# Optimization experiments

Measured on AMD Instinct MI355X. Metric: run time of the kernel, lower is better.

The kernel has to match this reference:

```python
import math
import jax, jax.numpy as jnp
import numpy as np

EMB = 1024
HEADS = 16
EXPAND = 2
HEAD_D = EMB // HEADS * EXPAND  # 128
N, S = 2, 2048


def setup_inputs() -> dict:
    key = jax.random.key(0)
    ks = jax.random.split(key, 10)
    lim = 1.0 / math.sqrt(EMB)  # nn.Linear default init range
    inp = {
        "query": jax.random.normal(ks[0], (N, S, EMB), dtype=jnp.float32),
        "key": jax.random.normal(ks[1], (N, S, EMB), dtype=jnp.float32),
        "value": jax.random.normal(ks[2], (N, S, EMB), dtype=jnp.float32),
        "mask": jax.random.randint(ks[3], (1, S, S), 0, 2, dtype=jnp.int32),
        "Wq": jax.random.uniform(ks[4], (EMB * EXPAND, EMB), jnp.float32, -lim, lim),
        "bq": jax.random.uniform(ks[5], (EMB * EXPAND,), jnp.float32, -lim, lim),
        "Wk": jax.random.uniform(ks[6], (EMB * EXPAND, EMB), jnp.float32, -lim, lim),
        "bk": jax.random.uniform(ks[7], (EMB * EXPAND,), jnp.float32, -lim, lim),
        "Wv": jax.random.uniform(ks[8], (EMB * EXPAND, EMB), jnp.float32, -lim, lim),
        "bv": jax.random.uniform(ks[9], (EMB * EXPAND,), jnp.float32, -lim, lim),
    }
    return inp


def _split_heads(x):
    # (N, S, H*D) -> (N, H, S, D)
    n, s, _ = x.shape
    return x.reshape(n, s, HEADS, HEAD_D).transpose(0, 2, 1, 3)


def reference(query, key, value, mask, Wq, bq, Wk, bk, Wv, bv):
    Q = _split_heads(jax.nn.relu(query @ Wq.T + bq))  # (N,H,S,D)
    K = _split_heads(jax.nn.relu(key @ Wk.T + bk))
    V = _split_heads(jax.nn.relu(value @ Wv.T + bv))
    scale = 1.0 / math.sqrt(HEAD_D)
    scores = jnp.einsum("nhqd,nhkd->nhqk", Q, K) * scale  # (N,H,S,S)
    scores = jnp.where(mask[None, :, :, :] == 0, jnp.float32(-1e7), scores)
    probs = jax.nn.softmax(scores, axis=-1)
    y = jnp.einsum("nhqk,nhkd->nhqd", probs, V)  # (N,H,S,D)
    return y.transpose(0, 2, 1, 3).reshape(query.shape[0], S, HEADS * HEAD_D)
```

## Files before the change

kernel.cpp:

```cpp
#include <hip/hip_runtime.h>

typedef __bf16 bf16;
typedef __bf16 bf16x8 __attribute__((ext_vector_type(8)));
typedef __bf16 bf16x4 __attribute__((ext_vector_type(4)));
typedef float f32x4 __attribute__((ext_vector_type(4)));

#define MFMA_BF16(A, B, C) __builtin_amdgcn_mfma_f32_16x16x32_bf16((A), (B), (C), 0, 0, 0)

#define EMB 1024
#define ODIM 2048
#define SEQ 2048
#define HEADS 16
#define HD 128

__device__ __forceinline__ void gload16(const bf16* g, const bf16* l) {
  __builtin_amdgcn_global_load_lds(
      (const __attribute__((address_space(1))) unsigned int*)(const void*)g,
      (__attribute__((address_space(3))) unsigned int*)(void*)l, 16, 0, 0);
}

__global__ __launch_bounds__(256) void cvt_bf16_k(const float* __restrict__ q,
                                                  const float* __restrict__ k,
                                                  const float* __restrict__ v,
                                                  const float* __restrict__ Wq,
                                                  const float* __restrict__ Wk,
                                                  const float* __restrict__ Wv,
                                                  bf16* __restrict__ Xall,
                                                  bf16* __restrict__ Wall) {
  const unsigned XV = 4096u * 1024u / 8u;
  const unsigned WV = 2048u * 1024u / 8u;
  unsigned id = blockIdx.x * 256 + threadIdx.x;
  const float* src;
  bf16* dst;
  size_t off;
  if (id < 3 * XV) {
    unsigned p = id / XV;
    off = (size_t)(id - p * XV) * 8;
    src = (p == 0) ? q : (p == 1 ? k : v);
    dst = Xall + (size_t)p * (4096u * 1024u);
  } else {
    unsigned id2 = id - 3 * XV;
    unsigned p = id2 / WV;
    off = (size_t)(id2 - p * WV) * 8;
    src = (p == 0) ? Wq : (p == 1 ? Wk : Wv);
    dst = Wall + (size_t)p * (2048u * 1024u);
  }
  float4 a = *(const float4*)(src + off);
  float4 b = *(const float4*)(src + off + 4);
  bf16x8 o;
  o[0] = (bf16)a.x; o[1] = (bf16)a.y; o[2] = (bf16)a.z; o[3] = (bf16)a.w;
  o[4] = (bf16)b.x; o[5] = (bf16)b.y; o[6] = (bf16)b.z; o[7] = (bf16)b.w;
  *(bf16x8*)(dst + off) = o;
}

__global__ __launch_bounds__(256) void build_maskbits_k(const int* __restrict__ mask,
                                                        unsigned long long* __restrict__ mb) {
  int w = blockIdx.x * 256 + threadIdx.x;
  int q = w >> 5, c = w & 31;
  const int4* m4 = reinterpret_cast<const int4*>(mask + (size_t)q * SEQ + c * 64);
  unsigned long long bits = 0ull;
#pragma unroll
  for (int i = 0; i < 16; ++i) {
    int4 v = m4[i];
    if (v.x) bits |= 1ull << (i * 4 + 0);
    if (v.y) bits |= 1ull << (i * 4 + 1);
    if (v.z) bits |= 1ull << (i * 4 + 2);
    if (v.w) bits |= 1ull << (i * 4 + 3);
  }
  mb[w] = bits;
}

__global__ __launch_bounds__(256) void proj_gemm_k(const bf16* __restrict__ Xall,
                                                   const bf16* __restrict__ Wall,
                                                   const float* __restrict__ bq,
                                                   const float* __restrict__ bk_,
                                                   const float* __restrict__ bv_,
                                                   bf16* __restrict__ Qb,
                                                   bf16* __restrict__ Kb,
                                                   bf16* __restrict__ Vt,
                                                   float qscale) {
  __shared__ union {
    struct { bf16 A[128 * 64]; bf16 B[128 * 64]; } s;
    bf16 C[128][136];
  } sm;

  const int t = threadIdx.x;
  const int lane = t & 63;
  const int wid = t >> 6;
  const int wm = wid >> 1, wn = wid & 1;
  const int lr = lane & 15, lg = lane >> 4;
  const int z = blockIdx.z;
  const int m0 = blockIdx.y * 128;
  const int n0 = blockIdx.x * 128;
  const bf16* X = Xall + (size_t)z * (4096u * 1024u);
  const bf16* W = Wall + (size_t)z * (2048u * 1024u);
  const float* bias = (z == 0) ? bq : (z == 1 ? bk_ : bv_);
  const float oscale = (z == 0) ? qscale : 1.0f;

  const int sr_ = t >> 3;
  const int scb = (t & 7) * 16;

  f32x4 acc[4][4];
#pragma unroll
  for (int i = 0; i < 4; ++i)
#pragma unroll
    for (int j = 0; j < 4; ++j) acc[i][j] = {0.f, 0.f, 0.f, 0.f};

  for (int k0 = 0; k0 < EMB; k0 += 64) {
#pragma unroll
    for (int j = 0; j < 4; ++j) {
      int r = j * 32 + sr_;
      int cb = scb ^ ((r & 7) << 4);
      gload16(X + (size_t)(m0 + r) * EMB + k0 + (cb >> 1), &sm.s.A[j * 2048 + t * 8]);
    }
#pragma unroll
    for (int j = 0; j < 4; ++j) {
      int r = j * 32 + sr_;
      int cb = scb ^ ((r & 7) << 4);
      gload16(W + (size_t)(n0 + r) * EMB + k0 + (cb >> 1), &sm.s.B[j * 2048 + t * 8]);
    }
    __syncthreads();

    bf16x8 af[4][2], bfr[4][2];
#pragma unroll
    for (int i = 0; i < 4; ++i)
#pragma unroll
      for (int s = 0; s < 2; ++s) {
        int ra = wm * 64 + i * 16 + lr;
        int ca = (s * 64 + lg * 16) ^ ((ra & 7) << 4);
        af[i][s] = *(const bf16x8*)&sm.s.A[ra * 64 + (ca >> 1)];
        int rb = wn * 64 + i * 16 + lr;
        int cb2 = (s * 64 + lg * 16) ^ ((rb & 7) << 4);
        bfr[i][s] = *(const bf16x8*)&sm.s.B[rb * 64 + (cb2 >> 1)];
      }
#pragma unroll
    for (int s = 0; s < 2; ++s)
#pragma unroll
      for (int mi = 0; mi < 4; ++mi)
#pragma unroll
        for (int ni = 0; ni < 4; ++ni)
          acc[mi][ni] = MFMA_BF16(af[mi][s], bfr[ni][s], acc[mi][ni]);
    __syncthreads();
  }

  float bv4[4];
#pragma unroll
  for (int ni = 0; ni < 4; ++ni) bv4[ni] = bias[n0 + wn * 64 + ni * 16 + lr];

  if (z < 2) {
    bf16* outN = (z == 0) ? Qb : Kb;
#pragma unroll
    for (int mi = 0; mi < 4; ++mi)
#pragma unroll
      for (int ni = 0; ni < 4; ++ni)
#pragma unroll
        for (int j = 0; j < 4; ++j) {
          float v = fmaxf(acc[mi][ni][j] + bv4[ni], 0.f) * oscale;
          int row = m0 + wm * 64 + mi * 16 + lg * 4 + j;
          int col = n0 + wn * 64 + ni * 16 + lr;
          outN[(size_t)row * ODIM + col] = (bf16)v;
        }
  } else {
#pragma unroll
    for (int mi = 0; mi < 4; ++mi)
#pragma unroll
      for (int ni = 0; ni < 4; ++ni)
#pragma unroll
        for (int j = 0; j < 4; ++j) {
          float v = fmaxf(acc[mi][ni][j] + bv4[ni], 0.f);
          int rit = wm * 64 + mi * 16 + lg * 4 + j;
          int cit = wn * 64 + ni * 16 + lr;
          sm.C[cit][rit] = (bf16)v;
        }
    __syncthreads();
    const int n = m0 >> 11;
    const int s0 = m0 & (SEQ - 1);
    const int h = blockIdx.x;
    bf16* base = Vt + ((size_t)(n * HEADS + h) * HD) * SEQ + s0;
#pragma unroll
    for (int i = 0; i < 8; ++i) {
      int cid = i * 256 + t;
      int d = cid >> 4, c = cid & 15;
      *(bf16x8*)(base + (size_t)d * SEQ + c * 8) = *(const bf16x8*)&sm.C[d][c * 8];
    }
  }
}


__device__ __forceinline__ int kswz(int r, int c) {
  int b = (r << 8) | (c << 1);
  b ^= (r & 7) << 4;
  return b >> 1;
}
__device__ __forceinline__ int vswz(int d, int s) {
  int b = (d << 7) | (s << 1);
  b ^= (d & 7) << 4;
  return b >> 1;
}

__global__ __launch_bounds__(512, 2) void attn_k(const bf16* __restrict__ Qb,
                                                 const bf16* __restrict__ Kb,
                                                 const bf16* __restrict__ Vt,
                                                 const unsigned long long* __restrict__ mb,
                                                 float* __restrict__ out) {
  __shared__ bf16 Ks[64 * 128];
  __shared__ bf16 Vs[128 * 64];
  __shared__ bf16 Ps[8][32][72];

  const int tid = threadIdx.x;
  const int lane = tid & 63;
  const int w = tid >> 6;
  const int lr = lane & 15, lg = lane >> 4;

  const int bid = blockIdx.x;
  const int swz = (bid & 7) * 32 + (bid >> 3);
  const int nh = swz >> 3;
  const int qt = swz & 7;
  const int n = nh >> 4, h = nh & 15;
  const int qrow = qt * 256 + w * 32;

  bf16x8 qf[2][4];
#pragma unroll
  for (int g = 0; g < 2; ++g) {
    const bf16* qp = Qb + (size_t)(n * SEQ + qrow + g * 16 + lr) * ODIM + h * HD + lg * 8;
#pragma unroll
    for (int ks = 0; ks < 4; ++ks) qf[g][ks] = *(const bf16x8*)(qp + ks * 32);
  }

  bf16x8 onesA;
  {
    bf16 o1 = (bf16)((lr == 0) ? 1.0f : 0.0f);
#pragma unroll
    for (int j = 0; j < 8; ++j) onesA[j] = o1;
  }

  const bf16* Kg = Kb + (size_t)(n * SEQ) * ODIM + h * HD;
  const bf16* Vg = Vt + (size_t)nh * HD * SEQ;

  const int rK = tid >> 4, cK = tid & 15;
  const int dV = tid >> 3, cV = tid & 7;
  const bf16* kgp = Kg + (size_t)rK * ODIM + cK * 8;
  const bf16* vgp = Vg + (size_t)dV * SEQ + cV * 8;

  bf16x8 kreg[2], vreg[2];
#pragma unroll
  for (int i = 0; i < 2; ++i) kreg[i] = *(const bf16x8*)(kgp + (size_t)i * 32 * ODIM);
#pragma unroll
  for (int i = 0; i < 2; ++i) vreg[i] = *(const bf16x8*)(vgp + (size_t)i * 64 * SEQ);
#pragma unroll
  for (int i = 0; i < 2; ++i) *(bf16x8*)&Ks[kswz(rK + i * 32, cK * 8)] = kreg[i];
#pragma unroll
  for (int i = 0; i < 2; ++i) *(bf16x8*)&Vs[vswz(dV + i * 64, cV * 8)] = vreg[i];
  __syncthreads();

  f32x4 oacc[2][9];
#pragma unroll
  for (int g = 0; g < 2; ++g)
#pragma unroll
    for (int i = 0; i < 9; ++i) oacc[g][i] = {0.f, 0.f, 0.f, 0.f};
  float mrun[2] = {-3.0e38f, -3.0e38f};

  const int NT = SEQ / 64;
  for (int kt = 0; kt < NT; ++kt) {
    if (kt + 1 < NT) {
      const bf16* kn = kgp + (size_t)(kt + 1) * 64 * ODIM;
      const bf16* vn = vgp + (size_t)(kt + 1) * 64;
#pragma unroll
      for (int i = 0; i < 2; ++i) kreg[i] = *(const bf16x8*)(kn + (size_t)i * 32 * ODIM);
#pragma unroll
      for (int i = 0; i < 2; ++i) vreg[i] = *(const bf16x8*)(vn + (size_t)i * 64 * SEQ);
    }

    unsigned long long mw0 = mb[(size_t)(qrow + lr) * 32 + kt];
    unsigned long long mw1 = mb[(size_t)(qrow + 16 + lr) * 32 + kt];

    f32x4 sacc[2][4];
#pragma unroll
    for (int f = 0; f < 4; ++f)
#pragma unroll
      for (int j = 0; j < 4; ++j) {
        int kk = f * 16 + lg * 4 + j;
        sacc[0][f][j] = ((mw0 >> kk) & 1ull) ? 0.f : -1.0e7f;
        sacc[1][f][j] = ((mw1 >> kk) & 1ull) ? 0.f : -1.0e7f;
      }
    __builtin_amdgcn_s_setprio(1);
#pragma unroll
    for (int f = 0; f < 4; ++f) {
#pragma unroll
      for (int ks = 0; ks < 4; ++ks) {
        bf16x8 kf = *(const bf16x8*)&Ks[kswz(f * 16 + lr, ks * 32 + lg * 8)];
        sacc[0][f] = MFMA_BF16(kf, qf[0][ks], sacc[0][f]);
        sacc[1][f] = MFMA_BF16(kf, qf[1][ks], sacc[1][f]);
      }
    }
    __builtin_amdgcn_s_setprio(0);

    float mt[2] = {-3.0e38f, -3.0e38f};
#pragma unroll
    for (int g = 0; g < 2; ++g) {
#pragma unroll
      for (int f = 0; f < 4; ++f) {
        float a = fmaxf(sacc[g][f][0], sacc[g][f][1]);
        float b = fmaxf(sacc[g][f][2], sacc[g][f][3]);
        mt[g] = fmaxf(mt[g], fmaxf(a, b));
      }
      mt[g] = fmaxf(mt[g], __shfl_xor(mt[g], 16));
      mt[g] = fmaxf(mt[g], __shfl_xor(mt[g], 32));
    }

    if (!__all((mt[0] <= mrun[0] + 8.0f) && (mt[1] <= mrun[1] + 8.0f))) {
#pragma unroll
      for (int g = 0; g < 2; ++g) {
        float mnew = fmaxf(mrun[g], mt[g]);
        float alpha = exp2f(mrun[g] - mnew);
        mrun[g] = mnew;
#pragma unroll
        for (int df = 0; df < 9; ++df)
#pragma unroll
          for (int j = 0; j < 4; ++j) oacc[g][df][j] *= alpha;
      }
    }

#pragma unroll
    for (int g = 0; g < 2; ++g)
#pragma unroll
      for (int f = 0; f < 4; ++f) {
        bf16x4 pw;
#pragma unroll
        for (int j = 0; j < 4; ++j) pw[j] = (bf16)exp2f(sacc[g][f][j] - mrun[g]);
        *(bf16x4*)&Ps[w][g * 16 + lr][f * 16 + lg * 4] = pw;
      }

    bf16x8 pB[2][2];
#pragma unroll
    for (int g = 0; g < 2; ++g)
#pragma unroll
      for (int ks = 0; ks < 2; ++ks)
        pB[g][ks] = *(const bf16x8*)&Ps[w][g * 16 + lr][ks * 32 + lg * 8];

    __builtin_amdgcn_s_setprio(1);
#pragma unroll
    for (int df = 0; df < 8; ++df) {
#pragma unroll
      for (int ks = 0; ks < 2; ++ks) {
        bf16x8 vf = *(const bf16x8*)&Vs[vswz(df * 16 + lr, ks * 32 + lg * 8)];
        oacc[0][df] = MFMA_BF16(vf, pB[0][ks], oacc[0][df]);
        oacc[1][df] = MFMA_BF16(vf, pB[1][ks], oacc[1][df]);
      }
    }
#pragma unroll
    for (int ks = 0; ks < 2; ++ks) {
      oacc[0][8] = MFMA_BF16(onesA, pB[0][ks], oacc[0][8]);
      oacc[1][8] = MFMA_BF16(onesA, pB[1][ks], oacc[1][8]);
    }
    __builtin_amdgcn_s_setprio(0);

    if (kt + 1 < NT) {
      __syncthreads();
#pragma unroll
      for (int i = 0; i < 2; ++i) *(bf16x8*)&Ks[kswz(rK + i * 32, cK * 8)] = kreg[i];
#pragma unroll
      for (int i = 0; i < 2; ++i) *(bf16x8*)&Vs[vswz(dV + i * 64, cV * 8)] = vreg[i];
      __syncthreads();
    }
  }

#pragma unroll
  for (int g = 0; g < 2; ++g) {
    float l = __shfl(oacc[g][8][0], lr);
    float inv = 1.0f / l;
    float* obase = out + (size_t)(n * SEQ + qrow + g * 16 + lr) * ODIM + h * HD;
#pragma unroll
    for (int df = 0; df < 8; ++df) {
      f32x4 o;
#pragma unroll
      for (int j = 0; j < 4; ++j) o[j] = oacc[g][df][j] * inv;
      *(f32x4*)(obase + df * 16 + lg * 4) = o;
    }
  }
}

extern "C" void kernel_launch(void* const* d_in, const int* in_sizes, int n_in,
                              void* d_out, int out_size, void* d_ws, size_t ws_size,
                              hipStream_t stream) {
  const float* q   = (const float*)d_in[0];
  const float* k   = (const float*)d_in[1];
  const float* v   = (const float*)d_in[2];
  const int*  mask = (const int*)d_in[3];
  const float* Wq  = (const float*)d_in[4];
  const float* bq  = (const float*)d_in[5];
  const float* Wk  = (const float*)d_in[6];
  const float* bk  = (const float*)d_in[7];
  const float* Wv  = (const float*)d_in[8];
  const float* bv  = (const float*)d_in[9];
  float* out = (float*)d_out;

  char* ws = (char*)d_ws;
  const size_t PLANE = (size_t)4096 * 2048 * sizeof(bf16);
  bf16* Qb = (bf16*)ws;
  bf16* Kb = (bf16*)(ws + PLANE);
  bf16* Vt = (bf16*)(ws + 2 * PLANE);
  unsigned long long* mb = (unsigned long long*)(ws + 3 * PLANE);
  bf16* Xall = (bf16*)(ws + 3 * PLANE + (4u << 20));
  bf16* Wall = (bf16*)(ws + 3 * PLANE + (4u << 20) + (size_t)3 * 4096 * 1024 * 2);

  const float qscale = 0.08838834764831845f * 1.4426950408889634f;

  cvt_bf16_k<<<9216, 256, 0, stream>>>(q, k, v, Wq, Wk, Wv, Xall, Wall);
  build_maskbits_k<<<256, 256, 0, stream>>>(mask, mb);
  proj_gemm_k<<<dim3(16, 32, 3), 256, 0, stream>>>(Xall, Wall, bq, bk, bv, Qb, Kb, Vt, qscale);
  attn_k<<<256, 512, 0, stream>>>(Qb, Kb, Vt, mb, out);
}
```

Measured before the change: 199.8 us.

## Software-pipeline QK^T one tile ahead with double-buffered K in attention

Restructures the attention loop so the QK^T MFMAs for the next key tile are issued before the softmax and PV of the current tile, with K held in a double-buffered LDS array loaded two tiles ahead. Blocks shrink from 512 to 256 threads (4 waves, 128 query rows) and the grid doubles to 512 so more blocks can be resident and spread across CUs. The aim is to overlap matrix work with the exp/max and LDS traffic. The cost is higher register pressure from holding two score accumulator sets and four K/V prefetch registers, plus more LDS per block and twice as many K/V reloads across the grid.

```diff
diff --git a/kernel.cpp b/kernel.cpp
--- a/kernel.cpp
+++ b/kernel.cpp
@@ -198,14 +198,14 @@
   return b >> 1;
 }
 
-__global__ __launch_bounds__(512, 2) void attn_k(const bf16* __restrict__ Qb,
+__global__ __launch_bounds__(256, 2) void attn_k(const bf16* __restrict__ Qb,
                                                  const bf16* __restrict__ Kb,
                                                  const bf16* __restrict__ Vt,
                                                  const unsigned long long* __restrict__ mb,
                                                  float* __restrict__ out) {
-  __shared__ bf16 Ks[64 * 128];
+  __shared__ bf16 Ks[2][64 * 128];
   __shared__ bf16 Vs[128 * 64];
-  __shared__ bf16 Ps[8][32][72];
+  __shared__ bf16 Ps[4][32][72];
 
   const int tid = threadIdx.x;
   const int lane = tid & 63;
@@ -213,11 +213,11 @@
   const int lr = lane & 15, lg = lane >> 4;
 
   const int bid = blockIdx.x;
-  const int swz = (bid & 7) * 32 + (bid >> 3);
-  const int nh = swz >> 3;
-  const int qt = swz & 7;
+  const int swz = (bid & 7) * 64 + (bid >> 3);
+  const int nh = swz >> 4;
+  const int qt = swz & 15;
   const int n = nh >> 4, h = nh & 15;
-  const int qrow = qt * 256 + w * 32;
+  const int qrow = qt * 128 + w * 32;
 
   bf16x8 qf[2][4];
 #pragma unroll
@@ -242,15 +242,20 @@
   const bf16* kgp = Kg + (size_t)rK * ODIM + cK * 8;
   const bf16* vgp = Vg + (size_t)dV * SEQ + cV * 8;
 
-  bf16x8 kreg[2], vreg[2];
-#pragma unroll
-  for (int i = 0; i < 2; ++i) kreg[i] = *(const bf16x8*)(kgp + (size_t)i * 32 * ODIM);
-#pragma unroll
-  for (int i = 0; i < 2; ++i) vreg[i] = *(const bf16x8*)(vgp + (size_t)i * 64 * SEQ);
-#pragma unroll
-  for (int i = 0; i < 2; ++i) *(bf16x8*)&Ks[kswz(rK + i * 32, cK * 8)] = kreg[i];
-#pragma unroll
-  for (int i = 0; i < 2; ++i) *(bf16x8*)&Vs[vswz(dV + i * 64, cV * 8)] = vreg[i];
+  bf16x8 kreg[4], vreg[4];
+
+#pragma unroll
+  for (int i = 0; i < 4; ++i) kreg[i] = *(const bf16x8*)(kgp + (size_t)(i * 16) * ODIM);
+#pragma unroll
+  for (int i = 0; i < 4; ++i) vreg[i] = *(const bf16x8*)(vgp + (size_t)(i * 32) * SEQ);
+#pragma unroll
+  for (int i = 0; i < 4; ++i) *(bf16x8*)&Ks[0][kswz(rK + i * 16, cK * 8)] = kreg[i];
+#pragma unroll
+  for (int i = 0; i < 4; ++i) *(bf16x8*)&Vs[vswz(dV + i * 32, cV * 8)] = vreg[i];
+#pragma unroll
+  for (int i = 0; i < 4; ++i) kreg[i] = *(const bf16x8*)(kgp + (size_t)(64 + i * 16) * ODIM);
+#pragma unroll
+  for (int i = 0; i < 4; ++i) *(bf16x8*)&Ks[1][kswz(rK + i * 16, cK * 8)] = kreg[i];
   __syncthreads();
 
   f32x4 oacc[2][9];
@@ -260,65 +265,76 @@
     for (int i = 0; i < 9; ++i) oacc[g][i] = {0.f, 0.f, 0.f, 0.f};
   float mrun[2] = {-3.0e38f, -3.0e38f};
 
-  const int NT = SEQ / 64;
-  for (int kt = 0; kt < NT; ++kt) {
-    if (kt + 1 < NT) {
-      const bf16* kn = kgp + (size_t)(kt + 1) * 64 * ODIM;
-      const bf16* vn = vgp + (size_t)(kt + 1) * 64;
-#pragma unroll
-      for (int i = 0; i < 2; ++i) kreg[i] = *(const bf16x8*)(kn + (size_t)i * 32 * ODIM);
-#pragma unroll
-      for (int i = 0; i < 2; ++i) vreg[i] = *(const bf16x8*)(vn + (size_t)i * 64 * SEQ);
-    }
-
-    unsigned long long mw0 = mb[(size_t)(qrow + lr) * 32 + kt];
-    unsigned long long mw1 = mb[(size_t)(qrow + 16 + lr) * 32 + kt];
-
-    f32x4 sacc[2][4];
+  f32x4 saccA[2][4], saccB[2][4];
+
+  auto qk = [&](int u, f32x4 (&sn)[2][4]) {
+    unsigned long long mw0 = mb[(size_t)(qrow + lr) * 32 + u];
+    unsigned long long mw1 = mb[(size_t)(qrow + 16 + lr) * 32 + u];
+    const bf16* Kst = Ks[u & 1];
 #pragma unroll
     for (int f = 0; f < 4; ++f)
 #pragma unroll
       for (int j = 0; j < 4; ++j) {
         int kk = f * 16 + lg * 4 + j;
-        sacc[0][f][j] = ((mw0 >> kk) & 1ull) ? 0.f : -1.0e7f;
-        sacc[1][f][j] = ((mw1 >> kk) & 1ull) ? 0.f : -1.0e7f;
+        sn[0][f][j] = ((mw0 >> kk) & 1ull) ? 0.f : -1.0e7f;
+        sn[1][f][j] = ((mw1 >> kk) & 1ull) ? 0.f : -1.0e7f;
       }
     __builtin_amdgcn_s_setprio(1);
 #pragma unroll
     for (int f = 0; f < 4; ++f) {
 #pragma unroll
       for (int ks = 0; ks < 4; ++ks) {
-        bf16x8 kf = *(const bf16x8*)&Ks[kswz(f * 16 + lr, ks * 32 + lg * 8)];
-        sacc[0][f] = MFMA_BF16(kf, qf[0][ks], sacc[0][f]);
-        sacc[1][f] = MFMA_BF16(kf, qf[1][ks], sacc[1][f]);
+        bf16x8 kf = *(const bf16x8*)&Kst[kswz(f * 16 + lr, ks * 32 + lg * 8)];
+        sn[0][f] = MFMA_BF16(kf, qf[0][ks], sn[0][f]);
+        sn[1][f] = MFMA_BF16(kf, qf[1][ks], sn[1][f]);
       }
     }
     __builtin_amdgcn_s_setprio(0);
-
-    float mt[2] = {-3.0e38f, -3.0e38f};
-#pragma unroll
-    for (int g = 0; g < 2; ++g) {
-#pragma unroll
-      for (int f = 0; f < 4; ++f) {
-        float a = fmaxf(sacc[g][f][0], sacc[g][f][1]);
-        float b = fmaxf(sacc[g][f][2], sacc[g][f][3]);
-        mt[g] = fmaxf(mt[g], fmaxf(a, b));
-      }
-      mt[g] = fmaxf(mt[g], __shfl_xor(mt[g], 16));
-      mt[g] = fmaxf(mt[g], __shfl_xor(mt[g], 32));
-    }
-
-    if (!__all((mt[0] <= mrun[0] + 8.0f) && (mt[1] <= mrun[1] + 8.0f))) {
-#pragma unroll
-      for (int g = 0; g < 2; ++g) {
-        float mnew = fmaxf(mrun[g], mt[g]);
-        float alpha = exp2f(mrun[g] - mnew);
-        mrun[g] = mnew;
-#pragma unroll
-        for (int df = 0; df < 9; ++df)
-#pragma unroll
-          for (int j = 0; j < 4; ++j) oacc[g][df][j] *= alpha;
-      }
+  };
+
+  qk(0, saccA);
+
+  const int NT = SEQ / 64;
+
+  auto body = [&](int t, f32x4 (&sc)[2][4], f32x4 (&sn)[2][4]) {
+    if (t + 2 < NT) {
+      const bf16* kn = kgp + (size_t)(t + 2) * 64 * ODIM;
+#pragma unroll
+      for (int i = 0; i < 4; ++i) kreg[i] = *(const bf16x8*)(kn + (size_t)(i * 16) * ODIM);
+    }
+    if (t + 1 < NT) {
+      const bf16* vn = vgp + (size_t)(t + 1) * 64;
+#pragma unroll
+      for (int i = 0; i < 4; ++i) vreg[i] = *(const bf16x8*)(vn + (size_t)(i * 32) * SEQ);
+    }
+
+    if (t + 1 < NT) qk(t + 1, sn);
+
+    float mt0 = -3.0e38f, mt1 = -3.0e38f;
+#pragma unroll
+    for (int f = 0; f < 4; ++f) {
+      mt0 = fmaxf(mt0, fmaxf(fmaxf(sc[0][f][0], sc[0][f][1]), fmaxf(sc[0][f][2], sc[0][f][3])));
+      mt1 = fmaxf(mt1, fmaxf(fmaxf(sc[1][f][0], sc[1][f][1]), fmaxf(sc[1][f][2], sc[1][f][3])));
+    }
+    mt0 = fmaxf(mt0, __shfl_xor(mt0, 16));
+    mt1 = fmaxf(mt1, __shfl_xor(mt1, 16));
+    mt0 = fmaxf(mt0, __shfl_xor(mt0, 32));
+    mt1 = fmaxf(mt1, __shfl_xor(mt1, 32));
+
+    if (!__all((mt0 <= mrun[0] + 8.0f) && (mt1 <= mrun[1] + 8.0f))) {
+      float m0n = fmaxf(mrun[0], mt0);
+      float m1n = fmaxf(mrun[1], mt1);
+      float a0 = exp2f(mrun[0] - m0n);
+      float a1 = exp2f(mrun[1] - m1n);
+      mrun[0] = m0n;
+      mrun[1] = m1n;
+#pragma unroll
+      for (int df = 0; df < 9; ++df)
+#pragma unroll
+        for (int j = 0; j < 4; ++j) {
+          oacc[0][df][j] *= a0;
+          oacc[1][df][j] *= a1;
+        }
     }
 
 #pragma unroll
@@ -327,7 +343,7 @@
       for (int f = 0; f < 4; ++f) {
         bf16x4 pw;
 #pragma unroll
-        for (int j = 0; j < 4; ++j) pw[j] = (bf16)exp2f(sacc[g][f][j] - mrun[g]);
+        for (int j = 0; j < 4; ++j) pw[j] = (bf16)exp2f(sc[g][f][j] - mrun[g]);
         *(bf16x4*)&Ps[w][g * 16 + lr][f * 16 + lg * 4] = pw;
       }
 
@@ -355,14 +371,21 @@
     }
     __builtin_amdgcn_s_setprio(0);
 
-    if (kt + 1 < NT) {
+    if (t + 1 < NT) {
       __syncthreads();
-#pragma unroll
-      for (int i = 0; i < 2; ++i) *(bf16x8*)&Ks[kswz(rK + i * 32, cK * 8)] = kreg[i];
-#pragma unroll
-      for (int i = 0; i < 2; ++i) *(bf16x8*)&Vs[vswz(dV + i * 64, cV * 8)] = vreg[i];
+      if (t + 2 < NT) {
+#pragma unroll
+        for (int i = 0; i < 4; ++i) *(bf16x8*)&Ks[t & 1][kswz(rK + i * 16, cK * 8)] = kreg[i];
+      }
+#pragma unroll
+      for (int i = 0; i < 4; ++i) *(bf16x8*)&Vs[vswz(dV + i * 32, cV * 8)] = vreg[i];
       __syncthreads();
     }
+  };
+
+  for (int kt = 0; kt < NT; kt += 2) {
+    body(kt, saccA, saccB);
+    body(kt + 1, saccB, saccA);
   }
 
 #pragma unroll
@@ -409,5 +432,5 @@
   cvt_bf16_k<<<9216, 256, 0, stream>>>(q, k, v, Wq, Wk, Wv, Xall, Wall);
   build_maskbits_k<<<256, 256, 0, stream>>>(mask, mb);
   proj_gemm_k<<<dim3(16, 32, 3), 256, 0, stream>>>(Xall, Wall, bq, bk, bv, Qb, Kb, Vt, qscale);
-  attn_k<<<256, 512, 0, stream>>>(Qb, Kb, Vt, mb, out);
-}
+  attn_k<<<512, 256, 0, stream>>>(Qb, Kb, Vt, mb, out);
+}
```

After: 497.9 us. 149% more time.

## Switch attention to 32x32x16 MFMA tiles with register row-sum and folded max

Applied to the files above, without the earlier changes.

Rewrites the attention inner loop to use 32x32x16 bf16 MFMA instructions instead of 16x16x32, so each wave handles its 32 query rows as one tile with 16-wide accumulators. The softmax denominator is now accumulated in registers rather than through an extra ones-matrix MFMA. The running max is folded into the score initialisation as an offset, and the LDS swizzles are reworked for the new access pattern. This cuts MFMA issue count and per-step shuffles, but raises register pressure and changes the LDS bank-conflict behaviour.

```diff
diff --git a/kernel.cpp b/kernel.cpp
--- a/kernel.cpp
+++ b/kernel.cpp
@@ -4,8 +4,10 @@
 typedef __bf16 bf16x8 __attribute__((ext_vector_type(8)));
 typedef __bf16 bf16x4 __attribute__((ext_vector_type(4)));
 typedef float f32x4 __attribute__((ext_vector_type(4)));
+typedef float f32x16 __attribute__((ext_vector_type(16)));
 
 #define MFMA_BF16(A, B, C) __builtin_amdgcn_mfma_f32_16x16x32_bf16((A), (B), (C), 0, 0, 0)
+#define MFMA32(A, B, C) __builtin_amdgcn_mfma_f32_32x32x16_bf16((A), (B), (C), 0, 0, 0)
 
 #define EMB 1024
 #define ODIM 2048
@@ -187,15 +189,11 @@
 }
 
 
-__device__ __forceinline__ int kswz(int r, int c) {
-  int b = (r << 8) | (c << 1);
-  b ^= (r & 7) << 4;
-  return b >> 1;
-}
-__device__ __forceinline__ int vswz(int d, int s) {
-  int b = (d << 7) | (s << 1);
-  b ^= (d & 7) << 4;
-  return b >> 1;
+__device__ __forceinline__ int kswz(int r, int cb) {
+  return (r * 256 + (cb ^ ((r & 15) << 4))) >> 1;
+}
+__device__ __forceinline__ int vswz(int r, int cb) {
+  return (r * 128 + (cb ^ ((r & 7) << 4))) >> 1;
 }
 
 __global__ __launch_bounds__(512, 2) void attn_k(const bf16* __restrict__ Qb,
@@ -210,7 +208,8 @@
   const int tid = threadIdx.x;
   const int lane = tid & 63;
   const int w = tid >> 6;
-  const int lr = lane & 15, lg = lane >> 4;
+  const int q31 = lane & 31;
+  const int hh = lane >> 5;
 
   const int bid = blockIdx.x;
   const int swz = (bid & 7) * 32 + (bid >> 3);
@@ -219,19 +218,11 @@
   const int n = nh >> 4, h = nh & 15;
   const int qrow = qt * 256 + w * 32;
 
-  bf16x8 qf[2][4];
-#pragma unroll
-  for (int g = 0; g < 2; ++g) {
-    const bf16* qp = Qb + (size_t)(n * SEQ + qrow + g * 16 + lr) * ODIM + h * HD + lg * 8;
-#pragma unroll
-    for (int ks = 0; ks < 4; ++ks) qf[g][ks] = *(const bf16x8*)(qp + ks * 32);
-  }
-
-  bf16x8 onesA;
+  bf16x8 qf[8];
   {
-    bf16 o1 = (bf16)((lr == 0) ? 1.0f : 0.0f);
-#pragma unroll
-    for (int j = 0; j < 8; ++j) onesA[j] = o1;
+    const bf16* qp = Qb + (size_t)(n * SEQ + qrow + q31) * ODIM + h * HD + hh * 8;
+#pragma unroll
+    for (int st = 0; st < 8; ++st) qf[st] = *(const bf16x8*)(qp + st * 16);
   }
 
   const bf16* Kg = Kb + (size_t)(n * SEQ) * ODIM + h * HD;
@@ -248,17 +239,18 @@
 #pragma unroll
   for (int i = 0; i < 2; ++i) vreg[i] = *(const bf16x8*)(vgp + (size_t)i * 64 * SEQ);
 #pragma unroll
-  for (int i = 0; i < 2; ++i) *(bf16x8*)&Ks[kswz(rK + i * 32, cK * 8)] = kreg[i];
-#pragma unroll
-  for (int i = 0; i < 2; ++i) *(bf16x8*)&Vs[vswz(dV + i * 64, cV * 8)] = vreg[i];
+  for (int i = 0; i < 2; ++i) *(bf16x8*)&Ks[kswz(rK + i * 32, cK * 16)] = kreg[i];
+#pragma unroll
+  for (int i = 0; i < 2; ++i) *(bf16x8*)&Vs[vswz(dV + i * 64, cV * 16)] = vreg[i];
   __syncthreads();
 
-  f32x4 oacc[2][9];
-#pragma unroll
-  for (int g = 0; g < 2; ++g)
-#pragma unroll
-    for (int i = 0; i < 9; ++i) oacc[g][i] = {0.f, 0.f, 0.f, 0.f};
-  float mrun[2] = {-3.0e38f, -3.0e38f};
+  f32x16 oacc[4];
+#pragma unroll
+  for (int i = 0; i < 4; ++i)
+#pragma unroll
+    for (int j = 0; j < 16; ++j) oacc[i][j] = 0.f;
+  float mrun = 0.f;
+  float lrun = 0.f;
 
   const int NT = SEQ / 64;
   for (int kt = 0; kt < NT; ++kt) {
@@ -271,113 +263,114 @@
       for (int i = 0; i < 2; ++i) vreg[i] = *(const bf16x8*)(vn + (size_t)i * 64 * SEQ);
     }
 
-    unsigned long long mw0 = mb[(size_t)(qrow + lr) * 32 + kt];
-    unsigned long long mw1 = mb[(size_t)(qrow + 16 + lr) * 32 + kt];
-
-    f32x4 sacc[2][4];
-#pragma unroll
-    for (int f = 0; f < 4; ++f)
+    unsigned long long mw = mb[(size_t)(qrow + q31) * 32 + kt];
+    unsigned w0 = (unsigned)(mw >> (4 * hh));
+    unsigned w1 = (unsigned)(mw >> (32 + 4 * hh));
+
+    f32x16 sacc[2];
+    float negm = -mrun;
+#pragma unroll
+    for (int rg = 0; rg < 4; ++rg)
 #pragma unroll
       for (int j = 0; j < 4; ++j) {
-        int kk = f * 16 + lg * 4 + j;
-        sacc[0][f][j] = ((mw0 >> kk) & 1ull) ? 0.f : -1.0e7f;
-        sacc[1][f][j] = ((mw1 >> kk) & 1ull) ? 0.f : -1.0e7f;
+        sacc[0][rg * 4 + j] = ((w0 >> (rg * 8 + j)) & 1u) ? negm : -1.0e7f;
+        sacc[1][rg * 4 + j] = ((w1 >> (rg * 8 + j)) & 1u) ? negm : -1.0e7f;
       }
     __builtin_amdgcn_s_setprio(1);
 #pragma unroll
-    for (int f = 0; f < 4; ++f) {
-#pragma unroll
-      for (int ks = 0; ks < 4; ++ks) {
-        bf16x8 kf = *(const bf16x8*)&Ks[kswz(f * 16 + lr, ks * 32 + lg * 8)];
-        sacc[0][f] = MFMA_BF16(kf, qf[0][ks], sacc[0][f]);
-        sacc[1][f] = MFMA_BF16(kf, qf[1][ks], sacc[1][f]);
+    for (int st = 0; st < 8; ++st) {
+      bf16x8 kf0 = *(const bf16x8*)&Ks[kswz(q31, st * 32 + hh * 16)];
+      bf16x8 kf1 = *(const bf16x8*)&Ks[kswz(32 + q31, st * 32 + hh * 16)];
+      sacc[0] = MFMA32(kf0, qf[st], sacc[0]);
+      sacc[1] = MFMA32(kf1, qf[st], sacc[1]);
+    }
+    __builtin_amdgcn_s_setprio(0);
+
+    float mt = -3.0e38f;
+#pragma unroll
+    for (int sub = 0; sub < 2; ++sub)
+#pragma unroll
+      for (int i = 0; i < 8; ++i) mt = fmaxf(mt, fmaxf(sacc[sub][2 * i], sacc[sub][2 * i + 1]));
+    mt = fmaxf(mt, __shfl_xor(mt, 32));
+
+    bf16x4 pk[2][4];
+    float lsum = 0.f;
+    if (!__all(mt <= 8.0f)) {
+      float d = fmaxf(mt, 0.f);
+      mrun += d;
+      float alpha = exp2f(-d);
+      lrun *= alpha;
+#pragma unroll
+      for (int i = 0; i < 4; ++i)
+#pragma unroll
+        for (int j = 0; j < 16; ++j) oacc[i][j] *= alpha;
+#pragma unroll
+      for (int sub = 0; sub < 2; ++sub)
+#pragma unroll
+        for (int rg = 0; rg < 4; ++rg)
+#pragma unroll
+          for (int j = 0; j < 4; ++j) {
+            float p = exp2f(sacc[sub][rg * 4 + j] - d);
+            lsum += p;
+            pk[sub][rg][j] = (bf16)p;
+          }
+    } else {
+#pragma unroll
+      for (int sub = 0; sub < 2; ++sub)
+#pragma unroll
+        for (int rg = 0; rg < 4; ++rg)
+#pragma unroll
+          for (int j = 0; j < 4; ++j) {
+            float p = exp2f(sacc[sub][rg * 4 + j]);
+            lsum += p;
+            pk[sub][rg][j] = (bf16)p;
+          }
+    }
+    lrun += lsum;
+
+#pragma unroll
+    for (int sub = 0; sub < 2; ++sub)
+#pragma unroll
+      for (int rg = 0; rg < 4; ++rg)
+        *(bf16x4*)&Ps[w][q31][sub * 32 + rg * 8 + 4 * hh] = pk[sub][rg];
+
+    bf16x8 pB[4];
+#pragma unroll
+    for (int st = 0; st < 4; ++st) pB[st] = *(const bf16x8*)&Ps[w][q31][st * 16 + hh * 8];
+
+    __builtin_amdgcn_s_setprio(1);
+#pragma unroll
+    for (int st = 0; st < 4; ++st) {
+#pragma unroll
+      for (int dsub = 0; dsub < 4; ++dsub) {
+        bf16x8 vf = *(const bf16x8*)&Vs[vswz(dsub * 32 + q31, st * 32 + hh * 16)];
+        oacc[dsub] = MFMA32(vf, pB[st], oacc[dsub]);
       }
-    }
-    __builtin_amdgcn_s_setprio(0);
-
-    float mt[2] = {-3.0e38f, -3.0e38f};
-#pragma unroll
-    for (int g = 0; g < 2; ++g) {
-#pragma unroll
-      for (int f = 0; f < 4; ++f) {
-        float a = fmaxf(sacc[g][f][0], sacc[g][f][1]);
-        float b = fmaxf(sacc[g][f][2], sacc[g][f][3]);
-        mt[g] = fmaxf(mt[g], fmaxf(a, b));
-      }
-      mt[g] = fmaxf(mt[g], __shfl_xor(mt[g], 16));
-      mt[g] = fmaxf(mt[g], __shfl_xor(mt[g], 32));
-    }
-
-    if (!__all((mt[0] <= mrun[0] + 8.0f) && (mt[1] <= mrun[1] + 8.0f))) {
-#pragma unroll
-      for (int g = 0; g < 2; ++g) {
-        float mnew = fmaxf(mrun[g], mt[g]);
-        float alpha = exp2f(mrun[g] - mnew);
-        mrun[g] = mnew;
-#pragma unroll
-        for (int df = 0; df < 9; ++df)
-#pragma unroll
-          for (int j = 0; j < 4; ++j) oacc[g][df][j] *= alpha;
-      }
-    }
-
-#pragma unroll
-    for (int g = 0; g < 2; ++g)
-#pragma unroll
-      for (int f = 0; f < 4; ++f) {
-        bf16x4 pw;
-#pragma unroll
-        for (int j = 0; j < 4; ++j) pw[j] = (bf16)exp2f(sacc[g][f][j] - mrun[g]);
-        *(bf16x4*)&Ps[w][g * 16 + lr][f * 16 + lg * 4] = pw;
-      }
-
-    bf16x8 pB[2][2];
-#pragma unroll
-    for (int g = 0; g < 2; ++g)
-#pragma unroll
-      for (int ks = 0; ks < 2; ++ks)
-        pB[g][ks] = *(const bf16x8*)&Ps[w][g * 16 + lr][ks * 32 + lg * 8];
-
-    __builtin_amdgcn_s_setprio(1);
-#pragma unroll
-    for (int df = 0; df < 8; ++df) {
-#pragma unroll
-      for (int ks = 0; ks < 2; ++ks) {
-        bf16x8 vf = *(const bf16x8*)&Vs[vswz(df * 16 + lr, ks * 32 + lg * 8)];
-        oacc[0][df] = MFMA_BF16(vf, pB[0][ks], oacc[0][df]);
-        oacc[1][df] = MFMA_BF16(vf, pB[1][ks], oacc[1][df]);
-      }
-    }
-#pragma unroll
-    for (int ks = 0; ks < 2; ++ks) {
-      oacc[0][8] = MFMA_BF16(onesA, pB[0][ks], oacc[0][8]);
-      oacc[1][8] = MFMA_BF16(onesA, pB[1][ks], oacc[1][8]);
     }
     __builtin_amdgcn_s_setprio(0);
 
     if (kt + 1 < NT) {
       __syncthreads();
 #pragma unroll
-      for (int i = 0; i < 2; ++i) *(bf16x8*)&Ks[kswz(rK + i * 32, cK * 8)] = kreg[i];
-#pragma unroll
-      for (int i = 0; i < 2; ++i) *(bf16x8*)&Vs[vswz(dV + i * 64, cV * 8)] = vreg[i];
+      for (int i = 0; i < 2; ++i) *(bf16x8*)&Ks[kswz(rK + i * 32, cK * 16)] = kreg[i];
+#pragma unroll
+      for (int i = 0; i < 2; ++i) *(bf16x8*)&Vs[vswz(dV + i * 64, cV * 16)] = vreg[i];
       __syncthreads();
     }
   }
 
-#pragma unroll
-  for (int g = 0; g < 2; ++g) {
-    float l = __shfl(oacc[g][8][0], lr);
-    float inv = 1.0f / l;
-    float* obase = out + (size_t)(n * SEQ + qrow + g * 16 + lr) * ODIM + h * HD;
-#pragma unroll
-    for (int df = 0; df < 8; ++df) {
+  float l = lrun + __shfl_xor(lrun, 32);
+  float inv = 1.0f / l;
+  float* ob = out + (size_t)(n * SEQ + qrow + q31) * ODIM + h * HD;
+#pragma unroll
+  for (int dsub = 0; dsub < 4; ++dsub)
+#pragma unroll
+    for (int rg = 0; rg < 4; ++rg) {
       f32x4 o;
 #pragma unroll
-      for (int j = 0; j < 4; ++j) o[j] = oacc[g][df][j] * inv;
-      *(f32x4*)(obase + df * 16 + lg * 4) = o;
-    }
-  }
+      for (int j = 0; j < 4; ++j) o[j] = oacc[dsub][rg * 4 + j] * inv;
+      *(f32x4*)(ob + dsub * 32 + rg * 8 + 4 * hh) = o;
+    }
 }
 
 extern "C" void kernel_launch(void* const* d_in, const int* in_sizes, int n_in,
```

After: 209.8 us. +5.0%, slower.

## Halve attention query tile per wave to launch twice as many blocks

Applied to the files above, without the earlier changes.

Each wave now handles 16 query rows instead of 32, so a block covers 128 queries and the grid doubles to 512 blocks. This gives better occupancy and fills all CUs on the MI355X (256 blocks could underfill 256 CUs with 2 blocks/CU allowed) and lowers register pressure. The cost is that each K/V tile loaded into LDS is reused by half as many query rows, which doubles global K/V traffic and the per-MFMA LDS read ratio.

```diff
diff --git a/kernel.cpp b/kernel.cpp
--- a/kernel.cpp
+++ b/kernel.cpp
@@ -205,7 +205,7 @@
                                                  float* __restrict__ out) {
   __shared__ bf16 Ks[64 * 128];
   __shared__ bf16 Vs[128 * 64];
-  __shared__ bf16 Ps[8][32][72];
+  __shared__ bf16 Ps[8][16][72];
 
   const int tid = threadIdx.x;
   const int lane = tid & 63;
@@ -213,18 +213,17 @@
   const int lr = lane & 15, lg = lane >> 4;
 
   const int bid = blockIdx.x;
-  const int swz = (bid & 7) * 32 + (bid >> 3);
-  const int nh = swz >> 3;
-  const int qt = swz & 7;
+  const int swz = (bid & 7) * 64 + (bid >> 3);
+  const int nh = swz >> 4;
+  const int qt = swz & 15;
   const int n = nh >> 4, h = nh & 15;
-  const int qrow = qt * 256 + w * 32;
-
-  bf16x8 qf[2][4];
-#pragma unroll
-  for (int g = 0; g < 2; ++g) {
-    const bf16* qp = Qb + (size_t)(n * SEQ + qrow + g * 16 + lr) * ODIM + h * HD + lg * 8;
-#pragma unroll
-    for (int ks = 0; ks < 4; ++ks) qf[g][ks] = *(const bf16x8*)(qp + ks * 32);
+  const int qrow = qt * 128 + w * 16;
+
+  bf16x8 qf[4];
+  {
+    const bf16* qp = Qb + (size_t)(n * SEQ + qrow + lr) * ODIM + h * HD + lg * 8;
+#pragma unroll
+    for (int ks = 0; ks < 4; ++ks) qf[ks] = *(const bf16x8*)(qp + ks * 32);
   }
 
   bf16x8 onesA;
@@ -253,12 +252,10 @@
   for (int i = 0; i < 2; ++i) *(bf16x8*)&Vs[vswz(dV + i * 64, cV * 8)] = vreg[i];
   __syncthreads();
 
-  f32x4 oacc[2][9];
-#pragma unroll
-  for (int g = 0; g < 2; ++g)
-#pragma unroll
-    for (int i = 0; i < 9; ++i) oacc[g][i] = {0.f, 0.f, 0.f, 0.f};
-  float mrun[2] = {-3.0e38f, -3.0e38f};
+  f32x4 oacc[9];
+#pragma unroll
+  for (int i = 0; i < 9; ++i) oacc[i] = {0.f, 0.f, 0.f, 0.f};
+  float mrun = -3.0e38f;
 
   const int NT = SEQ / 64;
   for (int kt = 0; kt < NT; ++kt) {
@@ -271,17 +268,15 @@
       for (int i = 0; i < 2; ++i) vreg[i] = *(const bf16x8*)(vn + (size_t)i * 64 * SEQ);
     }
 
-    unsigned long long mw0 = mb[(size_t)(qrow + lr) * 32 + kt];
-    unsigned long long mw1 = mb[(size_t)(qrow + 16 + lr) * 32 + kt];
-
-    f32x4 sacc[2][4];
+    unsigned long long mw = mb[(size_t)(qrow + lr) * 32 + kt];
+
+    f32x4 sacc[4];
 #pragma unroll
     for (int f = 0; f < 4; ++f)
 #pragma unroll
       for (int j = 0; j < 4; ++j) {
         int kk = f * 16 + lg * 4 + j;
-        sacc[0][f][j] = ((mw0 >> kk) & 1ull) ? 0.f : -1.0e7f;
-        sacc[1][f][j] = ((mw1 >> kk) & 1ull) ? 0.f : -1.0e7f;
+        sacc[f][j] = ((mw >> kk) & 1ull) ? 0.f : -1.0e7f;
       }
     __builtin_amdgcn_s_setprio(1);
 #pragma unroll
@@ -289,54 +284,43 @@
 #pragma unroll
       for (int ks = 0; ks < 4; ++ks) {
         bf16x8 kf = *(const bf16x8*)&Ks[kswz(f * 16 + lr, ks * 32 + lg * 8)];
-        sacc[0][f] = MFMA_BF16(kf, qf[0][ks], sacc[0][f]);
-        sacc[1][f] = MFMA_BF16(kf, qf[1][ks], sacc[1][f]);
+        sacc[f] = MFMA_BF16(kf, qf[ks], sacc[f]);
       }
     }
     __builtin_amdgcn_s_setprio(0);
 
-    float mt[2] = {-3.0e38f, -3.0e38f};
-#pragma unroll
-    for (int g = 0; g < 2; ++g) {
-#pragma unroll
-      for (int f = 0; f < 4; ++f) {
-        float a = fmaxf(sacc[g][f][0], sacc[g][f][1]);
-        float b = fmaxf(sacc[g][f][2], sacc[g][f][3]);
-        mt[g] = fmaxf(mt[g], fmaxf(a, b));
-      }
-      mt[g] = fmaxf(mt[g], __shfl_xor(mt[g], 16));
-      mt[g] = fmaxf(mt[g], __shfl_xor(mt[g], 32));
-    }
-
-    if (!__all((mt[0] <= mrun[0] + 8.0f) && (mt[1] <= mrun[1] + 8.0f))) {
-#pragma unroll
-      for (int g = 0; g < 2; ++g) {
-        float mnew = fmaxf(mrun[g], mt[g]);
-        float alpha = exp2f(mrun[g] - mnew);
-        mrun[g] = mnew;
-#pragma unroll
-        for (int df = 0; df < 9; ++df)
-#pragma unroll
-          for (int j = 0; j < 4; ++j) oacc[g][df][j] *= alpha;
-      }
-    }
-
-#pragma unroll
-    for (int g = 0; g < 2; ++g)
-#pragma unroll
-      for (int f = 0; f < 4; ++f) {
-        bf16x4 pw;
-#pragma unroll
-        for (int j = 0; j < 4; ++j) pw[j] = (bf16)exp2f(sacc[g][f][j] - mrun[g]);
-        *(bf16x4*)&Ps[w][g * 16 + lr][f * 16 + lg * 4] = pw;
-      }
-
-    bf16x8 pB[2][2];
-#pragma unroll
-    for (int g = 0; g < 2; ++g)
-#pragma unroll
-      for (int ks = 0; ks < 2; ++ks)
-        pB[g][ks] = *(const bf16x8*)&Ps[w][g * 16 + lr][ks * 32 + lg * 8];
+    float mt = -3.0e38f;
+#pragma unroll
+    for (int f = 0; f < 4; ++f) {
+      float a = fmaxf(sacc[f][0], sacc[f][1]);
+      float b = fmaxf(sacc[f][2], sacc[f][3]);
+      mt = fmaxf(mt, fmaxf(a, b));
+    }
+    mt = fmaxf(mt, __shfl_xor(mt, 16));
+    mt = fmaxf(mt, __shfl_xor(mt, 32));
+
+    if (!__all(mt <= mrun + 8.0f)) {
+      float mnew = fmaxf(mrun, mt);
+      float alpha = exp2f(mrun - mnew);
+      mrun = mnew;
+#pragma unroll
+      for (int df = 0; df < 9; ++df)
+#pragma unroll
+        for (int j = 0; j < 4; ++j) oacc[df][j] *= alpha;
+    }
+
+#pragma unroll
+    for (int f = 0; f < 4; ++f) {
+      bf16x4 pw;
+#pragma unroll
+      for (int j = 0; j < 4; ++j) pw[j] = (bf16)exp2f(sacc[f][j] - mrun);
+      *(bf16x4*)&Ps[w][lr][f * 16 + lg * 4] = pw;
+    }
+
+    bf16x8 pB[2];
+#pragma unroll
+    for (int ks = 0; ks < 2; ++ks)
+      pB[ks] = *(const bf16x8*)&Ps[w][lr][ks * 32 + lg * 8];
 
     __builtin_amdgcn_s_setprio(1);
 #pragma unroll
@@ -344,15 +328,11 @@
 #pragma unroll
       for (int ks = 0; ks < 2; ++ks) {
         bf16x8 vf = *(const bf16x8*)&Vs[vswz(df * 16 + lr, ks * 32 + lg * 8)];
-        oacc[0][df] = MFMA_BF16(vf, pB[0][ks], oacc[0][df]);
-        oacc[1][df] = MFMA_BF16(vf, pB[1][ks], oacc[1][df]);
+        oacc[df] = MFMA_BF16(vf, pB[ks], oacc[df]);
       }
     }
 #pragma unroll
-    for (int ks = 0; ks < 2; ++ks) {
-      oacc[0][8] = MFMA_BF16(onesA, pB[0][ks], oacc[0][8]);
-      oacc[1][8] = MFMA_BF16(onesA, pB[1][ks], oacc[1][8]);
-    }
+    for (int ks = 0; ks < 2; ++ks) oacc[8] = MFMA_BF16(onesA, pB[ks], oacc[8]);
     __builtin_amdgcn_s_setprio(0);
 
     if (kt + 1 < NT) {
@@ -365,16 +345,15 @@
     }
   }
 
-#pragma unroll
-  for (int g = 0; g < 2; ++g) {
-    float l = __shfl(oacc[g][8][0], lr);
+  {
+    float l = __shfl(oacc[8][0], lr);
     float inv = 1.0f / l;
-    float* obase = out + (size_t)(n * SEQ + qrow + g * 16 + lr) * ODIM + h * HD;
+    float* obase = out + (size_t)(n * SEQ + qrow + lr) * ODIM + h * HD;
 #pragma unroll
     for (int df = 0; df < 8; ++df) {
       f32x4 o;
 #pragma unroll
-      for (int j = 0; j < 4; ++j) o[j] = oacc[g][df][j] * inv;
+      for (int j = 0; j < 4; ++j) o[j] = oacc[df][j] * inv;
       *(f32x4*)(obase + df * 16 + lg * 4) = o;
     }
   }
@@ -409,5 +388,5 @@
   cvt_bf16_k<<<9216, 256, 0, stream>>>(q, k, v, Wq, Wk, Wv, Xall, Wall);
   build_maskbits_k<<<256, 256, 0, stream>>>(mask, mb);
   proj_gemm_k<<<dim3(16, 32, 3), 256, 0, stream>>>(Xall, Wall, bq, bk, bv, Qb, Kb, Vt, qscale);
-  attn_k<<<256, 512, 0, stream>>>(Qb, Kb, Vt, mb, out);
-}
+  attn_k<<<512, 512, 0, stream>>>(Qb, Kb, Vt, mb, out);
+}
```

Measured after the change: 233.6 us. 16.9% more time.
